# Kernel tuning notes

Measured on AMD Instinct MI355X. Metric: run time of the kernel, lower is better.

## Reference

```python
import jax, jax.numpy as jnp
import numpy as np

EMBED_DIM = 1024
NUM_HEADS = 16
HEAD_DIM = EMBED_DIM // NUM_HEADS


def setup_inputs() -> dict:
    key = jax.random.key(0)
    ks = jax.random.split(key, 11)
    B, S, E = 4, 2048, EMBED_DIM
    s = 1.0 / np.sqrt(E)
    return {
        "query": jax.random.normal(ks[0], (B, S, E), jnp.float32),
        "key": jax.random.normal(ks[1], (B, S, E), jnp.float32),
        "value": jax.random.normal(ks[2], (B, S, E), jnp.float32),
        "Wq": jax.random.normal(ks[3], (E, E), jnp.float32) * s,
        "bq": jnp.zeros((E,), jnp.float32),
        "Wk": jax.random.normal(ks[4], (E, E), jnp.float32) * s,
        "bk": jnp.zeros((E,), jnp.float32),
        "Wv": jax.random.normal(ks[5], (E, E), jnp.float32) * s,
        "bv": jnp.zeros((E,), jnp.float32),
        "Wo": jax.random.normal(ks[6], (E, E), jnp.float32) * s,
        "bo": jnp.zeros((E,), jnp.float32),
    }


def reference(query, key, value, Wq, bq, Wk, bk, Wv, bv, Wo, bo):
    B, S, E = query.shape
    H, D = NUM_HEADS, HEAD_DIM
    scale = jnp.float32(np.sqrt(D))
    # linear projections (torch Linear: x @ W.T + b)
    Q = (query @ Wq.T + bq).reshape(B, S, H, D).transpose(0, 2, 1, 3)  # [B,H,S,D]
    K = (key @ Wk.T + bk).reshape(B, S, H, D).transpose(0, 2, 1, 3)
    V = (value @ Wv.T + bv).reshape(B, S, H, D).transpose(0, 2, 1, 3)
    # full O(S^2) score materialization, matching the eager torch code
    scores = jnp.einsum("bhqd,bhkd->bhqk", Q, K) / scale  # [B,H,S,S]
    attn = jax.nn.softmax(scores, axis=-1)
    out = jnp.einsum("bhqk,bhkd->bhqd", attn, V)  # [B,H,S,D]
    out = out.transpose(0, 2, 1, 3).reshape(B, S, E)
    out = out @ Wo.T + bo
    return out, attn.mean(axis=1)
```

## Files before the change

kernel.cpp:

```cpp
#include <hip/hip_runtime.h>
#include <hip/hip_bf16.h>

#define DEVI __device__ __forceinline__

typedef __bf16 bf16x8 __attribute__((ext_vector_type(8)));
typedef __bf16 bf16x4 __attribute__((ext_vector_type(4)));
typedef float f32x4 __attribute__((ext_vector_type(4)));

constexpr int B_ = 4, S_ = 2048, E_ = 1024, H_ = 16, D_ = 64;
constexpr int N_ = B_ * S_;
constexpr float SCALE_ = 0.125f;

constexpr size_t XB_OFF = 0;
constexpr size_t WB_OFF = 50331648;
constexpr size_t QB_OFF = 58720256;
constexpr size_t KB_OFF = 75497472;
constexpr size_t VT_OFF = 92274688;
constexpr size_t CTX_OFF = 109051904;
constexpr size_t LS_OFF = 125829120;
constexpr size_t WS_NEED = 126353408;

typedef const __attribute__((address_space(1))) void* gas_ptr;
typedef __attribute__((address_space(3))) void* las_ptr;

DEVI void load_lds16(const void* g, void* l) {
  __builtin_amdgcn_global_load_lds((gas_ptr)g, (las_ptr)l, 16, 0, 0);
}

DEVI f32x4 mfma16(bf16x8 a, bf16x8 b, f32x4 c) {
  return __builtin_amdgcn_mfma_f32_16x16x32_bf16(a, b, c, 0, 0, 0);
}

__global__ __launch_bounds__(256) void conv_x(const float* __restrict__ q,
                                              const float* __restrict__ k,
                                              const float* __restrict__ v,
                                              __bf16* __restrict__ dst) {
  const float* src = (blockIdx.y == 0) ? q : ((blockIdx.y == 1) ? k : v);
  __bf16* d = dst + (size_t)blockIdx.y * N_ * E_;
  size_t i = ((size_t)blockIdx.x * blockDim.x + threadIdx.x) * 4;
  float4 f = *(const float4*)(src + i);
  bf16x4 o;
  o[0] = (__bf16)f.x; o[1] = (__bf16)f.y; o[2] = (__bf16)f.z; o[3] = (__bf16)f.w;
  *(bf16x4*)(d + i) = o;
}

__global__ __launch_bounds__(256) void conv_w(const float* __restrict__ wq,
                                              const float* __restrict__ wk,
                                              const float* __restrict__ wv,
                                              const float* __restrict__ wo,
                                              __bf16* __restrict__ dst) {
  const float* src = (blockIdx.y == 0) ? wq : ((blockIdx.y == 1) ? wk :
                     ((blockIdx.y == 2) ? wv : wo));
  __bf16* d = dst + (size_t)blockIdx.y * E_ * E_;
  size_t i = ((size_t)blockIdx.x * blockDim.x + threadIdx.x) * 4;
  float4 f = *(const float4*)(src + i);
  bf16x4 o;
  o[0] = (__bf16)f.x; o[1] = (__bf16)f.y; o[2] = (__bf16)f.z; o[3] = (__bf16)f.w;
  *(bf16x4*)(d + i) = o;
}

__global__ __launch_bounds__(256) void gemm_qkv(const __bf16* __restrict__ Xb,
                                                const __bf16* __restrict__ Wb,
                                                const float* __restrict__ bq,
                                                const float* __restrict__ bk,
                                                const float* __restrict__ bv,
                                                __bf16* __restrict__ Qb,
                                                __bf16* __restrict__ Kb,
                                                __bf16* __restrict__ Vt) {
  __shared__ __attribute__((aligned(16))) __bf16 As[128 * 32];
  __shared__ __attribute__((aligned(16))) __bf16 Bs[128 * 32];
  const int z = blockIdx.z;
  const __bf16* A = Xb + (size_t)z * N_ * E_;
  const __bf16* W = Wb + (size_t)z * E_ * E_;
  const float* bias = (z == 0) ? bq : ((z == 1) ? bk : bv);
  const int m0 = blockIdx.x * 128, n0 = blockIdx.y * 128;
  const int t = threadIdx.x, lane = t & 63, w = t >> 6;
  const int wm = w >> 1, wn = w & 1;

  f32x4 acc[4][4] = {};

  for (int kk = 0; kk < E_; kk += 32) {
#pragma unroll
    for (int i = 0; i < 2; ++i) {
      int c = t + i * 256;
      int row = c >> 2, kc = c & 3;
      load_lds16(A + (size_t)(m0 + row) * E_ + kk + kc * 8, (void*)(As + c * 8));
      load_lds16(W + (size_t)(n0 + row) * E_ + kk + kc * 8, (void*)(Bs + c * 8));
    }
    __syncthreads();
    bf16x8 a[4], b[4];
#pragma unroll
    for (int i = 0; i < 4; ++i)
      a[i] = *(const bf16x8*)(As + (wm * 64 + i * 16 + (lane & 15)) * 32 + ((lane >> 4) * 8));
#pragma unroll
    for (int j = 0; j < 4; ++j)
      b[j] = *(const bf16x8*)(Bs + (wn * 64 + j * 16 + (lane & 15)) * 32 + ((lane >> 4) * 8));
#pragma unroll
    for (int i = 0; i < 4; ++i)
#pragma unroll
      for (int j = 0; j < 4; ++j)
        acc[i][j] = mfma16(a[i], b[j], acc[i][j]);
    __syncthreads();
  }

#pragma unroll
  for (int i = 0; i < 4; ++i) {
    int mloc = wm * 64 + i * 16 + ((lane >> 4) << 2);
#pragma unroll
    for (int j = 0; j < 4; ++j) {
      int nloc = wn * 64 + j * 16 + (lane & 15);
      int n = n0 + nloc;
      int h = n >> 6, d = n & 63;
      float bs = bias[n];
      if (z == 2) {
        int m = m0 + mloc;
        int bb = m >> 11, s = m & 2047;
        bf16x4 pk;
#pragma unroll
        for (int r = 0; r < 4; ++r) pk[r] = (__bf16)(acc[i][j][r] + bs);
        *(bf16x4*)(Vt + ((size_t)(bb * H_ + h) * D_ + d) * S_ + s) = pk;
      } else {
        __bf16* dst = (z == 0) ? Qb : Kb;
#pragma unroll
        for (int r = 0; r < 4; ++r) {
          int m = m0 + mloc + r;
          int bb = m >> 11, s = m & 2047;
          dst[((size_t)(bb * H_ + h) * S_ + s) * D_ + d] = (__bf16)(acc[i][j][r] + bs);
        }
      }
    }
  }
}

__global__ __launch_bounds__(256, 4) void attn_pv(const __bf16* __restrict__ Qb,
                                                  const __bf16* __restrict__ Kb,
                                                  const __bf16* __restrict__ Vt,
                                                  float* __restrict__ Lsum,
                                                  __bf16* __restrict__ Ctx) {
  __shared__ __attribute__((aligned(16))) __bf16 Qs[2 * 128 * 32];
  __shared__ __attribute__((aligned(16))) __bf16 Ks[2 * 64 * 32];
  __shared__ __attribute__((aligned(16))) __bf16 Vs[2 * 64 * 32];

  const int q0 = blockIdx.x * 128;
  const int bh = blockIdx.y;
  const __bf16* Qh = Qb + (size_t)bh * S_ * D_;
  const __bf16* Kh = Kb + (size_t)bh * S_ * D_;
  const __bf16* Vh = Vt + (size_t)bh * D_ * S_;
  const int t = threadIdx.x, lane = t & 63, w = t >> 6;
  const int l15 = lane & 15, ghi8 = (lane >> 4) * 8;
  const int ksel = 8 * (l15 >> 2) + (l15 & 3);

#pragma unroll
  for (int i = 0; i < 4; ++i) {
    int c = t + i * 256;
    int sub = c >> 9, rem = c & 511, row = rem >> 2, kc = rem & 3;
    load_lds16(Qh + (size_t)(q0 + row) * D_ + sub * 32 + kc * 8, (void*)(Qs + c * 8));
  }
  __syncthreads();
  bf16x8 qf[2][2];
#pragma unroll
  for (int jb = 0; jb < 2; ++jb)
#pragma unroll
    for (int ks = 0; ks < 2; ++ks)
      qf[jb][ks] = *(const bf16x8*)(Qs + ks * 4096 + (w * 32 + jb * 16 + l15) * 32 + ghi8);

  bf16x8 ones;
#pragma unroll
  for (int i = 0; i < 8; ++i) ones[i] = (__bf16)1.0f;

  f32x4 acc[4][2] = {};
  f32x4 lacc[2] = {};

  for (int k0 = 0; k0 < S_; k0 += 64) {
#pragma unroll
    for (int i = 0; i < 2; ++i) {
      int c = t + i * 256;
      int sub = c >> 8, rem = c & 255, row = rem >> 2, kc = rem & 3;
      load_lds16(Kh + (size_t)(k0 + row) * D_ + sub * 32 + kc * 8, (void*)(Ks + c * 8));
      load_lds16(Vh + (size_t)row * S_ + k0 + sub * 32 + kc * 8, (void*)(Vs + c * 8));
    }
    __syncthreads();

#pragma unroll
    for (int chunk = 0; chunk < 2; ++chunk) {
      f32x4 sc[2][2];
#pragma unroll
      for (int blk = 0; blk < 2; ++blk) {
        int krow = chunk * 32 + 4 * blk + ksel;
        bf16x8 kf0 = *(const bf16x8*)(Ks + krow * 32 + ghi8);
        bf16x8 kf1 = *(const bf16x8*)(Ks + 2048 + krow * 32 + ghi8);
#pragma unroll
        for (int jb = 0; jb < 2; ++jb) {
          f32x4 s = {};
          s = mfma16(kf0, qf[jb][0], s);
          s = mfma16(kf1, qf[jb][1], s);
          sc[blk][jb] = s;
        }
      }
      bf16x8 pf[2];
#pragma unroll
      for (int jb = 0; jb < 2; ++jb) {
#pragma unroll
        for (int r = 0; r < 4; ++r) {
          pf[jb][r]     = (__bf16)__expf(sc[0][jb][r] * SCALE_);
          pf[jb][4 + r] = (__bf16)__expf(sc[1][jb][r] * SCALE_);
        }
        lacc[jb] = mfma16(ones, pf[jb], lacc[jb]);
      }
#pragma unroll
      for (int mb = 0; mb < 4; ++mb) {
        bf16x8 vf = *(const bf16x8*)(Vs + chunk * 2048 + (mb * 16 + l15) * 32 + ghi8);
#pragma unroll
        for (int jb = 0; jb < 2; ++jb)
          acc[mb][jb] = mfma16(vf, pf[jb], acc[mb][jb]);
      }
    }
    __syncthreads();
  }

  if (lane < 16) {
#pragma unroll
    for (int jb = 0; jb < 2; ++jb)
      Lsum[(size_t)bh * S_ + q0 + w * 32 + jb * 16 + lane] = lacc[jb][0];
  }

  const int bb = bh >> 4, h = bh & 15;
#pragma unroll
  for (int jb = 0; jb < 2; ++jb) {
    float invl = 1.0f / lacc[jb][0];
    int q = q0 + w * 32 + jb * 16 + l15;
#pragma unroll
    for (int mb = 0; mb < 4; ++mb) {
      int d = mb * 16 + ((lane >> 4) << 2);
      bf16x4 pk;
#pragma unroll
      for (int r = 0; r < 4; ++r) pk[r] = (__bf16)(acc[mb][jb][r] * invl);
      *(bf16x4*)(Ctx + ((size_t)bb * S_ + q) * E_ + h * 64 + d) = pk;
    }
  }
}

__global__ __launch_bounds__(256, 4) void attn_mean(const __bf16* __restrict__ Qb,
                                                    const __bf16* __restrict__ Kb,
                                                    const float* __restrict__ Lsum,
                                                    float* __restrict__ meanout) {
  __shared__ __attribute__((aligned(16))) __bf16 Qs[2 * 128 * 32];
  __shared__ __attribute__((aligned(16))) __bf16 Ks2[2 * 128 * 32];
  const int k0 = blockIdx.x * 128, q0 = blockIdx.y * 128, bI = blockIdx.z;
  const int t = threadIdx.x, lane = t & 63, w = t >> 6;
  const int l15 = lane & 15, ghi8 = (lane >> 4) * 8;
  const int ksel = 8 * (l15 >> 2) + (l15 & 3);

  f32x4 macc[4][2][2] = {};

  for (int h = 0; h < H_; ++h) {
    const size_t bh = (size_t)bI * H_ + h;
    const __bf16* Qh = Qb + bh * S_ * D_;
    const __bf16* Kh = Kb + bh * S_ * D_;
#pragma unroll
    for (int i = 0; i < 4; ++i) {
      int c = t + i * 256;
      int sub = c >> 9, rem = c & 511, row = rem >> 2, kc = rem & 3;
      load_lds16(Qh + (size_t)(q0 + row) * D_ + sub * 32 + kc * 8, (void*)(Qs + c * 8));
      load_lds16(Kh + (size_t)(k0 + row) * D_ + sub * 32 + kc * 8, (void*)(Ks2 + c * 8));
    }
    float invl[2];
#pragma unroll
    for (int jb = 0; jb < 2; ++jb)
      invl[jb] = 1.0f / Lsum[bh * S_ + q0 + w * 32 + jb * 16 + l15];
    __syncthreads();

    bf16x8 qf[2][2];
#pragma unroll
    for (int jb = 0; jb < 2; ++jb)
#pragma unroll
      for (int ks = 0; ks < 2; ++ks)
        qf[jb][ks] = *(const bf16x8*)(Qs + ks * 4096 + (w * 32 + jb * 16 + l15) * 32 + ghi8);

#pragma unroll
    for (int chunk = 0; chunk < 4; ++chunk) {
#pragma unroll
      for (int blk = 0; blk < 2; ++blk) {
        int krow = chunk * 32 + 4 * blk + ksel;
        bf16x8 kf0 = *(const bf16x8*)(Ks2 + krow * 32 + ghi8);
        bf16x8 kf1 = *(const bf16x8*)(Ks2 + 4096 + krow * 32 + ghi8);
#pragma unroll
        for (int jb = 0; jb < 2; ++jb) {
          f32x4 s = {};
          s = mfma16(kf0, qf[jb][0], s);
          s = mfma16(kf1, qf[jb][1], s);
#pragma unroll
          for (int r = 0; r < 4; ++r)
            macc[chunk][blk][jb][r] += __expf(s[r] * SCALE_) * invl[jb];
        }
      }
    }
    __syncthreads();
  }

#pragma unroll
  for (int chunk = 0; chunk < 4; ++chunk)
#pragma unroll
    for (int blk = 0; blk < 2; ++blk)
#pragma unroll
      for (int jb = 0; jb < 2; ++jb) {
        int q = q0 + w * 32 + jb * 16 + l15;
        int kb = k0 + chunk * 32 + 8 * (lane >> 4) + 4 * blk;
        f32x4 o;
#pragma unroll
        for (int r = 0; r < 4; ++r) o[r] = macc[chunk][blk][jb][r] * 0.0625f;
        *(f32x4*)(meanout + ((size_t)bI * S_ + q) * S_ + kb) = o;
      }
}

__global__ __launch_bounds__(256) void gemm_out(const __bf16* __restrict__ Ctx,
                                                const __bf16* __restrict__ Wo,
                                                const float* __restrict__ bo,
                                                float* __restrict__ out) {
  __shared__ __attribute__((aligned(16))) __bf16 As[128 * 32];
  __shared__ __attribute__((aligned(16))) __bf16 Bs[128 * 32];
  const int m0 = blockIdx.x * 128, n0 = blockIdx.y * 128;
  const int t = threadIdx.x, lane = t & 63, w = t >> 6;
  const int wm = w >> 1, wn = w & 1;

  f32x4 acc[4][4] = {};

  for (int kk = 0; kk < E_; kk += 32) {
#pragma unroll
    for (int i = 0; i < 2; ++i) {
      int c = t + i * 256;
      int row = c >> 2, kc = c & 3;
      load_lds16(Ctx + (size_t)(m0 + row) * E_ + kk + kc * 8, (void*)(As + c * 8));
      load_lds16(Wo + (size_t)(n0 + row) * E_ + kk + kc * 8, (void*)(Bs + c * 8));
    }
    __syncthreads();
    bf16x8 a[4], b[4];
#pragma unroll
    for (int i = 0; i < 4; ++i)
      a[i] = *(const bf16x8*)(As + (wm * 64 + i * 16 + (lane & 15)) * 32 + ((lane >> 4) * 8));
#pragma unroll
    for (int j = 0; j < 4; ++j)
      b[j] = *(const bf16x8*)(Bs + (wn * 64 + j * 16 + (lane & 15)) * 32 + ((lane >> 4) * 8));
#pragma unroll
    for (int i = 0; i < 4; ++i)
#pragma unroll
      for (int j = 0; j < 4; ++j)
        acc[i][j] = mfma16(a[i], b[j], acc[i][j]);
    __syncthreads();
  }

#pragma unroll
  for (int i = 0; i < 4; ++i) {
    int mloc = wm * 64 + i * 16 + ((lane >> 4) << 2);
#pragma unroll
    for (int j = 0; j < 4; ++j) {
      int n = n0 + wn * 64 + j * 16 + (lane & 15);
      float bs = bo[n];
#pragma unroll
      for (int r = 0; r < 4; ++r)
        out[(size_t)(m0 + mloc + r) * E_ + n] = acc[i][j][r] + bs;
    }
  }
}

extern "C" void kernel_launch(void* const* d_in, const int* in_sizes, int n_in,
                              void* d_out, int out_size, void* d_ws, size_t ws_size,
                              hipStream_t stream) {
  if (ws_size < WS_NEED) {
    hipMemsetAsync(d_out, 0, (size_t)out_size * sizeof(float), stream);
    return;
  }

  const float* q  = (const float*)d_in[0];
  const float* k  = (const float*)d_in[1];
  const float* v  = (const float*)d_in[2];
  const float* Wq = (const float*)d_in[3];
  const float* bq = (const float*)d_in[4];
  const float* Wk = (const float*)d_in[5];
  const float* bk = (const float*)d_in[6];
  const float* Wv = (const float*)d_in[7];
  const float* bv = (const float*)d_in[8];
  const float* Wo = (const float*)d_in[9];
  const float* bo = (const float*)d_in[10];

  char* ws = (char*)d_ws;
  __bf16* Xb  = (__bf16*)(ws + XB_OFF);
  __bf16* Wb  = (__bf16*)(ws + WB_OFF);
  __bf16* Qb  = (__bf16*)(ws + QB_OFF);
  __bf16* Kb  = (__bf16*)(ws + KB_OFF);
  __bf16* Vt  = (__bf16*)(ws + VT_OFF);
  __bf16* Ctx = (__bf16*)(ws + CTX_OFF);
  float*  Ls  = (float*)(ws + LS_OFF);

  float* out0 = (float*)d_out;
  float* out1 = (float*)d_out + (size_t)N_ * E_;

  conv_x<<<dim3(N_ * E_ / 4 / 256, 3), 256, 0, stream>>>(q, k, v, Xb);
  conv_w<<<dim3(E_ * E_ / 4 / 256, 4), 256, 0, stream>>>(Wq, Wk, Wv, Wo, Wb);
  gemm_qkv<<<dim3(N_ / 128, E_ / 128, 3), 256, 0, stream>>>(Xb, Wb, bq, bk, bv, Qb, Kb, Vt);
  attn_pv<<<dim3(S_ / 128, B_ * H_), 256, 0, stream>>>(Qb, Kb, Vt, Ls, Ctx);
  attn_mean<<<dim3(S_ / 128, S_ / 128, B_), 256, 0, stream>>>(Qb, Kb, Ls, out1);
  gemm_out<<<dim3(N_ / 128, E_ / 128), 256, 0, stream>>>(Ctx, Wb + 3 * (size_t)E_ * E_, bo, out0);
}
```

Baseline: 439.3 us.

## Swizzle LDS tiles to avoid bank conflicts and use native exp2 in softmax

```diff
diff --git a/kernel.cpp b/kernel.cpp
--- a/kernel.cpp
+++ b/kernel.cpp
@@ -9,7 +9,7 @@
 
 constexpr int B_ = 4, S_ = 2048, E_ = 1024, H_ = 16, D_ = 64;
 constexpr int N_ = B_ * S_;
-constexpr float SCALE_ = 0.125f;
+constexpr float SC2_ = 0.18033688011112042f;
 
 constexpr size_t XB_OFF = 0;
 constexpr size_t WB_OFF = 50331648;
@@ -30,6 +30,14 @@
 DEVI f32x4 mfma16(bf16x8 a, bf16x8 b, f32x4 c) {
   return __builtin_amdgcn_mfma_f32_16x16x32_bf16(a, b, c, 0, 0, 0);
 }
+
+DEVI int swz(int row) { return ((row >> 1) ^ (row >> 3)) & 3; }
+
+#if __has_builtin(__builtin_amdgcn_exp2f)
+DEVI float ex2(float x) { return __builtin_amdgcn_exp2f(x); }
+#else
+DEVI float ex2(float x) { return exp2f(x); }
+#endif
 
 __global__ __launch_bounds__(256) void conv_x(const float* __restrict__ q,
                                               const float* __restrict__ k,
@@ -76,6 +84,7 @@
   const int m0 = blockIdx.x * 128, n0 = blockIdx.y * 128;
   const int t = threadIdx.x, lane = t & 63, w = t >> 6;
   const int wm = w >> 1, wn = w & 1;
+  const int l15 = lane & 15, g = lane >> 4;
 
   f32x4 acc[4][4] = {};
 
@@ -84,17 +93,22 @@
     for (int i = 0; i < 2; ++i) {
       int c = t + i * 256;
       int row = c >> 2, kc = c & 3;
-      load_lds16(A + (size_t)(m0 + row) * E_ + kk + kc * 8, (void*)(As + c * 8));
-      load_lds16(W + (size_t)(n0 + row) * E_ + kk + kc * 8, (void*)(Bs + c * 8));
+      int sl = kc ^ swz(row);
+      load_lds16(A + (size_t)(m0 + row) * E_ + kk + sl * 8, (void*)(As + c * 8));
+      load_lds16(W + (size_t)(n0 + row) * E_ + kk + sl * 8, (void*)(Bs + c * 8));
     }
     __syncthreads();
     bf16x8 a[4], b[4];
 #pragma unroll
-    for (int i = 0; i < 4; ++i)
-      a[i] = *(const bf16x8*)(As + (wm * 64 + i * 16 + (lane & 15)) * 32 + ((lane >> 4) * 8));
-#pragma unroll
-    for (int j = 0; j < 4; ++j)
-      b[j] = *(const bf16x8*)(Bs + (wn * 64 + j * 16 + (lane & 15)) * 32 + ((lane >> 4) * 8));
+    for (int i = 0; i < 4; ++i) {
+      int row = wm * 64 + i * 16 + l15;
+      a[i] = *(const bf16x8*)(As + row * 32 + (g ^ swz(row)) * 8);
+    }
+#pragma unroll
+    for (int j = 0; j < 4; ++j) {
+      int row = wn * 64 + j * 16 + l15;
+      b[j] = *(const bf16x8*)(Bs + row * 32 + (g ^ swz(row)) * 8);
+    }
 #pragma unroll
     for (int i = 0; i < 4; ++i)
 #pragma unroll
@@ -105,10 +119,10 @@
 
 #pragma unroll
   for (int i = 0; i < 4; ++i) {
-    int mloc = wm * 64 + i * 16 + ((lane >> 4) << 2);
+    int mloc = wm * 64 + i * 16 + (g << 2);
 #pragma unroll
     for (int j = 0; j < 4; ++j) {
-      int nloc = wn * 64 + j * 16 + (lane & 15);
+      int nloc = wn * 64 + j * 16 + l15;
       int n = n0 + nloc;
       int h = n >> 6, d = n & 63;
       float bs = bias[n];
@@ -147,22 +161,25 @@
   const __bf16* Kh = Kb + (size_t)bh * S_ * D_;
   const __bf16* Vh = Vt + (size_t)bh * D_ * S_;
   const int t = threadIdx.x, lane = t & 63, w = t >> 6;
-  const int l15 = lane & 15, ghi8 = (lane >> 4) * 8;
+  const int l15 = lane & 15, g = lane >> 4;
   const int ksel = 8 * (l15 >> 2) + (l15 & 3);
 
 #pragma unroll
   for (int i = 0; i < 4; ++i) {
     int c = t + i * 256;
     int sub = c >> 9, rem = c & 511, row = rem >> 2, kc = rem & 3;
-    load_lds16(Qh + (size_t)(q0 + row) * D_ + sub * 32 + kc * 8, (void*)(Qs + c * 8));
+    int sl = kc ^ swz(row);
+    load_lds16(Qh + (size_t)(q0 + row) * D_ + sub * 32 + sl * 8, (void*)(Qs + c * 8));
   }
   __syncthreads();
   bf16x8 qf[2][2];
 #pragma unroll
-  for (int jb = 0; jb < 2; ++jb)
+  for (int jb = 0; jb < 2; ++jb) {
+    int row = w * 32 + jb * 16 + l15;
 #pragma unroll
     for (int ks = 0; ks < 2; ++ks)
-      qf[jb][ks] = *(const bf16x8*)(Qs + ks * 4096 + (w * 32 + jb * 16 + l15) * 32 + ghi8);
+      qf[jb][ks] = *(const bf16x8*)(Qs + ks * 4096 + row * 32 + (g ^ swz(row)) * 8);
+  }
 
   bf16x8 ones;
 #pragma unroll
@@ -176,8 +193,9 @@
     for (int i = 0; i < 2; ++i) {
       int c = t + i * 256;
       int sub = c >> 8, rem = c & 255, row = rem >> 2, kc = rem & 3;
-      load_lds16(Kh + (size_t)(k0 + row) * D_ + sub * 32 + kc * 8, (void*)(Ks + c * 8));
-      load_lds16(Vh + (size_t)row * S_ + k0 + sub * 32 + kc * 8, (void*)(Vs + c * 8));
+      int sl = kc ^ swz(row);
+      load_lds16(Kh + (size_t)(k0 + row) * D_ + sub * 32 + sl * 8, (void*)(Ks + c * 8));
+      load_lds16(Vh + (size_t)row * S_ + k0 + sub * 32 + sl * 8, (void*)(Vs + c * 8));
     }
     __syncthreads();
 
@@ -187,8 +205,9 @@
 #pragma unroll
       for (int blk = 0; blk < 2; ++blk) {
         int krow = chunk * 32 + 4 * blk + ksel;
-        bf16x8 kf0 = *(const bf16x8*)(Ks + krow * 32 + ghi8);
-        bf16x8 kf1 = *(const bf16x8*)(Ks + 2048 + krow * 32 + ghi8);
+        int so = (g ^ swz(krow)) * 8;
+        bf16x8 kf0 = *(const bf16x8*)(Ks + krow * 32 + so);
+        bf16x8 kf1 = *(const bf16x8*)(Ks + 2048 + krow * 32 + so);
 #pragma unroll
         for (int jb = 0; jb < 2; ++jb) {
           f32x4 s = {};
@@ -202,14 +221,15 @@
       for (int jb = 0; jb < 2; ++jb) {
 #pragma unroll
         for (int r = 0; r < 4; ++r) {
-          pf[jb][r]     = (__bf16)__expf(sc[0][jb][r] * SCALE_);
-          pf[jb][4 + r] = (__bf16)__expf(sc[1][jb][r] * SCALE_);
+          pf[jb][r]     = (__bf16)ex2(sc[0][jb][r] * SC2_);
+          pf[jb][4 + r] = (__bf16)ex2(sc[1][jb][r] * SC2_);
         }
         lacc[jb] = mfma16(ones, pf[jb], lacc[jb]);
       }
 #pragma unroll
       for (int mb = 0; mb < 4; ++mb) {
-        bf16x8 vf = *(const bf16x8*)(Vs + chunk * 2048 + (mb * 16 + l15) * 32 + ghi8);
+        int row = mb * 16 + l15;
+        bf16x8 vf = *(const bf16x8*)(Vs + chunk * 2048 + row * 32 + (g ^ swz(row)) * 8);
 #pragma unroll
         for (int jb = 0; jb < 2; ++jb)
           acc[mb][jb] = mfma16(vf, pf[jb], acc[mb][jb]);
@@ -231,7 +251,7 @@
     int q = q0 + w * 32 + jb * 16 + l15;
 #pragma unroll
     for (int mb = 0; mb < 4; ++mb) {
-      int d = mb * 16 + ((lane >> 4) << 2);
+      int d = mb * 16 + (g << 2);
       bf16x4 pk;
 #pragma unroll
       for (int r = 0; r < 4; ++r) pk[r] = (__bf16)(acc[mb][jb][r] * invl);
@@ -248,7 +268,7 @@
   __shared__ __attribute__((aligned(16))) __bf16 Ks2[2 * 128 * 32];
   const int k0 = blockIdx.x * 128, q0 = blockIdx.y * 128, bI = blockIdx.z;
   const int t = threadIdx.x, lane = t & 63, w = t >> 6;
-  const int l15 = lane & 15, ghi8 = (lane >> 4) * 8;
+  const int l15 = lane & 15, g = lane >> 4;
   const int ksel = 8 * (l15 >> 2) + (l15 & 3);
 
   f32x4 macc[4][2][2] = {};
@@ -261,8 +281,9 @@
     for (int i = 0; i < 4; ++i) {
       int c = t + i * 256;
       int sub = c >> 9, rem = c & 511, row = rem >> 2, kc = rem & 3;
-      load_lds16(Qh + (size_t)(q0 + row) * D_ + sub * 32 + kc * 8, (void*)(Qs + c * 8));
-      load_lds16(Kh + (size_t)(k0 + row) * D_ + sub * 32 + kc * 8, (void*)(Ks2 + c * 8));
+      int sl = kc ^ swz(row);
+      load_lds16(Qh + (size_t)(q0 + row) * D_ + sub * 32 + sl * 8, (void*)(Qs + c * 8));
+      load_lds16(Kh + (size_t)(k0 + row) * D_ + sub * 32 + sl * 8, (void*)(Ks2 + c * 8));
     }
     float invl[2];
 #pragma unroll
@@ -272,18 +293,21 @@
 
     bf16x8 qf[2][2];
 #pragma unroll
-    for (int jb = 0; jb < 2; ++jb)
+    for (int jb = 0; jb < 2; ++jb) {
+      int row = w * 32 + jb * 16 + l15;
 #pragma unroll
       for (int ks = 0; ks < 2; ++ks)
-        qf[jb][ks] = *(const bf16x8*)(Qs + ks * 4096 + (w * 32 + jb * 16 + l15) * 32 + ghi8);
+        qf[jb][ks] = *(const bf16x8*)(Qs + ks * 4096 + row * 32 + (g ^ swz(row)) * 8);
+    }
 
 #pragma unroll
     for (int chunk = 0; chunk < 4; ++chunk) {
 #pragma unroll
       for (int blk = 0; blk < 2; ++blk) {
         int krow = chunk * 32 + 4 * blk + ksel;
-        bf16x8 kf0 = *(const bf16x8*)(Ks2 + krow * 32 + ghi8);
-        bf16x8 kf1 = *(const bf16x8*)(Ks2 + 4096 + krow * 32 + ghi8);
+        int so = (g ^ swz(krow)) * 8;
+        bf16x8 kf0 = *(const bf16x8*)(Ks2 + krow * 32 + so);
+        bf16x8 kf1 = *(const bf16x8*)(Ks2 + 4096 + krow * 32 + so);
 #pragma unroll
         for (int jb = 0; jb < 2; ++jb) {
           f32x4 s = {};
@@ -291,7 +315,7 @@
           s = mfma16(kf1, qf[jb][1], s);
 #pragma unroll
           for (int r = 0; r < 4; ++r)
-            macc[chunk][blk][jb][r] += __expf(s[r] * SCALE_) * invl[jb];
+            macc[chunk][blk][jb][r] += ex2(s[r] * SC2_) * invl[jb];
         }
       }
     }
@@ -305,7 +329,7 @@
 #pragma unroll
       for (int jb = 0; jb < 2; ++jb) {
         int q = q0 + w * 32 + jb * 16 + l15;
-        int kb = k0 + chunk * 32 + 8 * (lane >> 4) + 4 * blk;
+        int kb = k0 + chunk * 32 + 8 * g + 4 * blk;
         f32x4 o;
 #pragma unroll
         for (int r = 0; r < 4; ++r) o[r] = macc[chunk][blk][jb][r] * 0.0625f;
@@ -322,6 +346,7 @@
   const int m0 = blockIdx.x * 128, n0 = blockIdx.y * 128;
   const int t = threadIdx.x, lane = t & 63, w = t >> 6;
   const int wm = w >> 1, wn = w & 1;
+  const int l15 = lane & 15, g = lane >> 4;
 
   f32x4 acc[4][4] = {};
 
@@ -330,17 +355,22 @@
     for (int i = 0; i < 2; ++i) {
       int c = t + i * 256;
       int row = c >> 2, kc = c & 3;
-      load_lds16(Ctx + (size_t)(m0 + row) * E_ + kk + kc * 8, (void*)(As + c * 8));
-      load_lds16(Wo + (size_t)(n0 + row) * E_ + kk + kc * 8, (void*)(Bs + c * 8));
+      int sl = kc ^ swz(row);
+      load_lds16(Ctx + (size_t)(m0 + row) * E_ + kk + sl * 8, (void*)(As + c * 8));
+      load_lds16(Wo + (size_t)(n0 + row) * E_ + kk + sl * 8, (void*)(Bs + c * 8));
     }
     __syncthreads();
     bf16x8 a[4], b[4];
 #pragma unroll
-    for (int i = 0; i < 4; ++i)
-      a[i] = *(const bf16x8*)(As + (wm * 64 + i * 16 + (lane & 15)) * 32 + ((lane >> 4) * 8));
-#pragma unroll
-    for (int j = 0; j < 4; ++j)
-      b[j] = *(const bf16x8*)(Bs + (wn * 64 + j * 16 + (lane & 15)) * 32 + ((lane >> 4) * 8));
+    for (int i = 0; i < 4; ++i) {
+      int row = wm * 64 + i * 16 + l15;
+      a[i] = *(const bf16x8*)(As + row * 32 + (g ^ swz(row)) * 8);
+    }
+#pragma unroll
+    for (int j = 0; j < 4; ++j) {
+      int row = wn * 64 + j * 16 + l15;
+      b[j] = *(const bf16x8*)(Bs + row * 32 + (g ^ swz(row)) * 8);
+    }
 #pragma unroll
     for (int i = 0; i < 4; ++i)
 #pragma unroll
@@ -351,10 +381,10 @@
 
 #pragma unroll
   for (int i = 0; i < 4; ++i) {
-    int mloc = wm * 64 + i * 16 + ((lane >> 4) << 2);
+    int mloc = wm * 64 + i * 16 + (g << 2);
 #pragma unroll
     for (int j = 0; j < 4; ++j) {
-      int n = n0 + wn * 64 + j * 16 + (lane & 15);
+      int n = n0 + wn * 64 + j * 16 + l15;
       float bs = bo[n];
 #pragma unroll
       for (int r = 0; r < 4; ++r)
```

New measurement: 435.4 us. Within noise of the previous version (-0.9%).
